# Kernel tuning notes

Measured on AMD Instinct MI355X. Metric: run time of the kernel, lower is better.

The kernel has to match this reference:

```python
import jax, jax.numpy as jnp
import numpy as np

N_NODES = 100000
N_EDGES = 1600000
MOTIF_DIM = 32
HIDDEN = 64


def setup_inputs() -> dict:
    key = jax.random.key(0)
    k1, k2, k3, k4 = jax.random.split(key, 4)
    motif_x = jax.random.normal(k1, (N_NODES, MOTIF_DIM), dtype=jnp.float32)
    edge_index = jax.random.randint(k2, (2, N_EDGES), 0, N_NODES, dtype=jnp.int64)
    in_dim = 4 * MOTIF_DIM
    W1 = jax.random.normal(k3, (in_dim, HIDDEN), dtype=jnp.float32) / np.sqrt(in_dim)
    b1 = jnp.zeros((HIDDEN,), dtype=jnp.float32)
    W2 = jax.random.normal(k4, (HIDDEN, 1), dtype=jnp.float32) / np.sqrt(HIDDEN)
    b2 = jnp.zeros((1,), dtype=jnp.float32)
    return {"motif_x": motif_x, "edge_index": edge_index, "W1": W1, "b1": b1, "W2": W2, "b2": b2}


def reference(motif_x, edge_index, W1, b1, W2, b2):
    src = edge_index[0]
    dst = edge_index[1]
    mu = motif_x[src]                      # [E, D] gather
    mv = motif_x[dst]                      # [E, D] gather
    feats = jnp.concatenate([mu, mv, jnp.abs(mu - mv), mu * mv], axis=1)  # [E, 4D]
    h = jax.nn.relu(feats @ W1 + b1)       # [E, H]
    g = jax.nn.sigmoid(h @ W2 + b2)[:, 0]  # [E]
    return jnp.clip(g, 0.0, 1.0)
```

## Files before the change

### kernel.cpp

```cpp
#include <hip/hip_runtime.h>

#define D 32
#define H 64

typedef __attribute__((ext_vector_type(8))) short bf16x8;
typedef __attribute__((ext_vector_type(4))) float f32x4;

union AB { uint4 u; bf16x8 v; };

__device__ __forceinline__ short f2bf_s(float f) {
  unsigned u = __float_as_uint(f);
  u += 0x7fffu + ((u >> 16) & 1u);
  return (short)(u >> 16);
}

__device__ __forceinline__ unsigned pack_bf2(float lo, float hi) {
  return __builtin_amdgcn_perm(__float_as_uint(hi), __float_as_uint(lo), 0x07060302u);
}

__global__ __launch_bounds__(256) void prep(
    const float* __restrict__ x, const float* __restrict__ W1,
    short* __restrict__ xbf, short* __restrict__ btab, int n4, int nPack) {
  int b = blockIdx.x;
  if (b < nPack) {
    int i = b * 256 + threadIdx.x;
    if (i < n4) {
      float4 v = ((const float4*)x)[i];
      short4 o;
      o.x = f2bf_s(v.x); o.y = f2bf_s(v.y); o.z = f2bf_s(v.z); o.w = f2bf_s(v.w);
      ((short4*)xbf)[i] = o;
    }
  } else {
    int id = (b - nPack) * 256 + threadIdx.x;
    if (id < 16 * 64 * 8) {
      int j = id & 7;
      int l = (id >> 3) & 63;
      int f = id >> 9;
      int s = f & 3, t = f >> 2;
      int k = s * 32 + (l >> 4) * 8 + j;
      int n = t * 16 + (l & 15);
      btab[id] = f2bf_s(W1[k * H + n]);
    }
  }
}

__device__ __forceinline__ void gather_tile(
    const uint4* __restrict__ xb, const int* __restrict__ ei,
    int tile, int m, int q, int nE, int nTiles, uint4& mu, uint4& mv) {
  int tc = tile < nTiles ? tile : nTiles - 1;
  int e  = tc * 16 + m;
  int ec = e < nE ? e : nE - 1;
  int s  = ei[ec];
  int d  = ei[ec + nE];
  mu = xb[s * 4 + q];
  mv = xb[d * 4 + q];
}

__device__ __forceinline__ void compute_tile(
    uint4 muU, uint4 mvU, const bf16x8* __restrict__ B,
    const f32x4* __restrict__ bias, const float* __restrict__ w2v, float bias2,
    int tile, int q, int m, int nE, float* __restrict__ out) {
  AB mu, mv, ac, ap;
  mu.u = muU; mv.u = mvU;
#pragma unroll
  for (int k = 0; k < 4; ++k) {
    unsigned a = (&mu.u.x)[k], b = (&mv.u.x)[k];
    float alo = __uint_as_float(a << 16);
    float ahi = __uint_as_float(a & 0xffff0000u);
    float blo = __uint_as_float(b << 16);
    float bhi = __uint_as_float(b & 0xffff0000u);
    float dlo = alo - blo, dhi = ahi - bhi;
    (&ac.u.x)[k] = pack_bf2(dlo, dhi) & 0x7fff7fffu;
    (&ap.u.x)[k] = pack_bf2(alo * blo, ahi * bhi);
  }

  float part[4];
#pragma unroll
  for (int t = 0; t < 4; ++t) {
    f32x4 acc = bias[t];
    acc = __builtin_amdgcn_mfma_f32_16x16x32_bf16(mu.v, B[t * 4 + 0], acc, 0, 0, 0);
    acc = __builtin_amdgcn_mfma_f32_16x16x32_bf16(mv.v, B[t * 4 + 1], acc, 0, 0, 0);
    acc = __builtin_amdgcn_mfma_f32_16x16x32_bf16(ac.v, B[t * 4 + 2], acc, 0, 0, 0);
    acc = __builtin_amdgcn_mfma_f32_16x16x32_bf16(ap.v, B[t * 4 + 3], acc, 0, 0, 0);
#pragma unroll
    for (int r = 0; r < 4; ++r) {
      float h = fmaxf(acc[r], 0.f);
      part[r] = (t == 0) ? h * w2v[0] : fmaf(h, w2v[t], part[r]);
    }
  }

#pragma unroll
  for (int mask = 1; mask < 16; mask <<= 1)
#pragma unroll
    for (int r = 0; r < 4; ++r)
      part[r] += __shfl_xor(part[r], mask, 64);

  if (m < 4) {
    int ew = tile * 16 + q * 4 + m;
    if (ew < nE) {
      float z = part[m] + bias2;
      float g = 1.f / (1.f + __expf(-z));
      out[ew] = fminf(fmaxf(g, 0.f), 1.f);
    }
  }
}

__global__ __launch_bounds__(256) void edge_mfma(
    const short* __restrict__ xbf, const short* __restrict__ btab,
    const int* __restrict__ ei,
    const float* __restrict__ b1, const float* __restrict__ W2,
    const float* __restrict__ b2, float* __restrict__ out,
    int nE, int nTiles) {
  int lane = threadIdx.x & 63;
  int wid  = (blockIdx.x * 256 + threadIdx.x) >> 6;
  int nW   = (gridDim.x * 256) >> 6;
  int m = lane & 15;
  int q = lane >> 4;

  bf16x8 B[16];
#pragma unroll
  for (int f = 0; f < 16; ++f)
    B[f] = *(const bf16x8*)(btab + (f * 64 + lane) * 8);

  f32x4 bias[4];
  float w2v[4];
#pragma unroll
  for (int t = 0; t < 4; ++t) {
    float bv = b1[t * 16 + m];
    bias[t] = (f32x4){bv, bv, bv, bv};
    w2v[t] = W2[t * 16 + m];
  }
  float bias2 = b2[0];

  const uint4* xb = (const uint4*)xbf;

  int t0 = wid, t1 = wid + nW;
  uint4 mu0, mv0, mu1, mv1;
  gather_tile(xb, ei, t0, m, q, nE, nTiles, mu0, mv0);
  gather_tile(xb, ei, t1, m, q, nE, nTiles, mu1, mv1);

  while (t0 < nTiles) {
    int n0 = t0 + 2 * nW, n1 = t1 + 2 * nW;
    uint4 pmu0, pmv0, pmu1, pmv1;
    gather_tile(xb, ei, n0, m, q, nE, nTiles, pmu0, pmv0);
    gather_tile(xb, ei, n1, m, q, nE, nTiles, pmu1, pmv1);

    compute_tile(mu0, mv0, B, bias, w2v, bias2, t0, q, m, nE, out);
    compute_tile(mu1, mv1, B, bias, w2v, bias2, t1, q, m, nE, out);

    mu0 = pmu0; mv0 = pmv0; mu1 = pmu1; mv1 = pmv1;
    t0 = n0; t1 = n1;
  }
}

__global__ __launch_bounds__(256) void edge_full(
    const float* __restrict__ x, const int* __restrict__ ei,
    const float* __restrict__ W1, const float* __restrict__ b1,
    const float* __restrict__ W2, const float* __restrict__ b2,
    float* __restrict__ out, int nE) {
  int e = blockIdx.x * 256 + threadIdx.x;
  if (e >= nE) return;
  int s = ei[e];
  int d = ei[e + nE];
  const float4* mu4 = (const float4*)(x + (size_t)s * D);
  const float4* mv4 = (const float4*)(x + (size_t)d * D);
  float mu[D], mv[D], c[D], p[D];
#pragma unroll
  for (int qq = 0; qq < D / 4; ++qq) {
    float4 a = mu4[qq];
    float4 b = mv4[qq];
    mu[4*qq+0] = a.x; mv[4*qq+0] = b.x; c[4*qq+0] = fabsf(a.x-b.x); p[4*qq+0] = a.x*b.x;
    mu[4*qq+1] = a.y; mv[4*qq+1] = b.y; c[4*qq+1] = fabsf(a.y-b.y); p[4*qq+1] = a.y*b.y;
    mu[4*qq+2] = a.z; mv[4*qq+2] = b.z; c[4*qq+2] = fabsf(a.z-b.z); p[4*qq+2] = a.z*b.z;
    mu[4*qq+3] = a.w; mv[4*qq+3] = b.w; c[4*qq+3] = fabsf(a.w-b.w); p[4*qq+3] = a.w*b.w;
  }
  float z = b2[0];
  for (int j = 0; j < H; ++j) {
    float a = b1[j];
#pragma unroll
    for (int k = 0; k < D; ++k) {
      a = fmaf(mu[k], W1[k * H + j], a);
      a = fmaf(mv[k], W1[(D + k) * H + j], a);
      a = fmaf(c[k],  W1[(2 * D + k) * H + j], a);
      a = fmaf(p[k],  W1[(3 * D + k) * H + j], a);
    }
    a = fmaxf(a, 0.f);
    z = fmaf(a, W2[j], z);
  }
  float g = 1.f / (1.f + __expf(-z));
  out[e] = fminf(fmaxf(g, 0.f), 1.f);
}

extern "C" void kernel_launch(void* const* d_in, const int* in_sizes, int n_in,
                              void* d_out, int out_size, void* d_ws, size_t ws_size,
                              hipStream_t stream) {
  const float* x  = (const float*)d_in[0];
  const int*   ei = (const int*)d_in[1];
  const float* W1 = (const float*)d_in[2];
  const float* b1 = (const float*)d_in[3];
  const float* W2 = (const float*)d_in[4];
  const float* b2 = (const float*)d_in[5];
  float* out = (float*)d_out;

  int nN = in_sizes[0] / D;
  int nE = in_sizes[1] / 2;

  size_t xbf_shorts = (size_t)nN * D;
  size_t need = (xbf_shorts + 16 * 64 * 8) * sizeof(short);
  if (ws_size >= need) {
    short* xbf  = (short*)d_ws;
    short* btab = xbf + xbf_shorts;
    int n4 = nN * D / 4;
    int nPack = (n4 + 255) / 256;
    int nBt = (16 * 64 * 8 + 255) / 256;
    prep<<<nPack + nBt, 256, 0, stream>>>(x, W1, xbf, btab, n4, nPack);
    int nTiles = (nE + 15) / 16;
    edge_mfma<<<2048, 256, 0, stream>>>(xbf, btab, ei, b1, W2, b2, out, nE, nTiles);
  } else {
    edge_full<<<(nE + 255) / 256, 256, 0, stream>>>(x, ei, W1, b1, W2, b2, out, nE);
  }
}
```

Measured before the change: 128.5 us.

## Restructure edge gather into 4-tile chunks with two-stage index/feature prefetch

Each wave now processes chunks of four 16-edge tiles. Edge indices are prefetched two chunks ahead and node features one chunk ahead, and each tile's feature loads are reissued right after that tile's compute. The aim is to keep more independent gathers in flight and to hide the dependent index-then-feature load latency. It also drops the redundant clamp after the sigmoid, keeps bias as scalars to save registers, and exits waves with no work early. The cost is higher register pressure from the 4-deep buffers, which may lower occupancy.

```diff
diff --git a/kernel.cpp b/kernel.cpp
--- a/kernel.cpp
+++ b/kernel.cpp
@@ -44,21 +44,9 @@
   }
 }
 
-__device__ __forceinline__ void gather_tile(
-    const uint4* __restrict__ xb, const int* __restrict__ ei,
-    int tile, int m, int q, int nE, int nTiles, uint4& mu, uint4& mv) {
-  int tc = tile < nTiles ? tile : nTiles - 1;
-  int e  = tc * 16 + m;
-  int ec = e < nE ? e : nE - 1;
-  int s  = ei[ec];
-  int d  = ei[ec + nE];
-  mu = xb[s * 4 + q];
-  mv = xb[d * 4 + q];
-}
-
 __device__ __forceinline__ void compute_tile(
     uint4 muU, uint4 mvU, const bf16x8* __restrict__ B,
-    const f32x4* __restrict__ bias, const float* __restrict__ w2v, float bias2,
+    const float* __restrict__ b1v, const float* __restrict__ w2v, float bias2,
     int tile, int q, int m, int nE, float* __restrict__ out) {
   AB mu, mv, ac, ap;
   mu.u = muU; mv.u = mvU;
@@ -77,7 +65,8 @@
   float part[4];
 #pragma unroll
   for (int t = 0; t < 4; ++t) {
-    f32x4 acc = bias[t];
+    float bv = b1v[t];
+    f32x4 acc = (f32x4){bv, bv, bv, bv};
     acc = __builtin_amdgcn_mfma_f32_16x16x32_bf16(mu.v, B[t * 4 + 0], acc, 0, 0, 0);
     acc = __builtin_amdgcn_mfma_f32_16x16x32_bf16(mv.v, B[t * 4 + 1], acc, 0, 0, 0);
     acc = __builtin_amdgcn_mfma_f32_16x16x32_bf16(ac.v, B[t * 4 + 2], acc, 0, 0, 0);
@@ -99,8 +88,7 @@
     int ew = tile * 16 + q * 4 + m;
     if (ew < nE) {
       float z = part[m] + bias2;
-      float g = 1.f / (1.f + __expf(-z));
-      out[ew] = fminf(fmaxf(g, 0.f), 1.f);
+      out[ew] = 1.f / (1.f + __expf(-z));
     }
   }
 }
@@ -116,40 +104,69 @@
   int nW   = (gridDim.x * 256) >> 6;
   int m = lane & 15;
   int q = lane >> 4;
+  int nChunks = (nTiles + 3) >> 2;
+  if (wid >= nChunks) return;
 
   bf16x8 B[16];
 #pragma unroll
   for (int f = 0; f < 16; ++f)
     B[f] = *(const bf16x8*)(btab + (f * 64 + lane) * 8);
 
-  f32x4 bias[4];
-  float w2v[4];
-#pragma unroll
-  for (int t = 0; t < 4; ++t) {
-    float bv = b1[t * 16 + m];
-    bias[t] = (f32x4){bv, bv, bv, bv};
+  float b1v[4], w2v[4];
+#pragma unroll
+  for (int t = 0; t < 4; ++t) {
+    b1v[t] = b1[t * 16 + m];
     w2v[t] = W2[t * 16 + m];
   }
   float bias2 = b2[0];
 
   const uint4* xb = (const uint4*)xbf;
-
-  int t0 = wid, t1 = wid + nW;
-  uint4 mu0, mv0, mu1, mv1;
-  gather_tile(xb, ei, t0, m, q, nE, nTiles, mu0, mv0);
-  gather_tile(xb, ei, t1, m, q, nE, nTiles, mu1, mv1);
-
-  while (t0 < nTiles) {
-    int n0 = t0 + 2 * nW, n1 = t1 + 2 * nW;
-    uint4 pmu0, pmv0, pmu1, pmv1;
-    gather_tile(xb, ei, n0, m, q, nE, nTiles, pmu0, pmv0);
-    gather_tile(xb, ei, n1, m, q, nE, nTiles, pmu1, pmv1);
-
-    compute_tile(mu0, mv0, B, bias, w2v, bias2, t0, q, m, nE, out);
-    compute_tile(mu1, mv1, B, bias, w2v, bias2, t1, q, m, nE, out);
-
-    mu0 = pmu0; mv0 = pmv0; mu1 = pmu1; mv1 = pmv1;
-    t0 = n0; t1 = n1;
+  int eLim = nE - 1;
+  int cLim = nChunks - 1;
+
+  int sn[4], dn[4], s2[4], d2[4];
+  uint4 amu[4], amv[4];
+
+  int c = wid;
+#pragma unroll
+  for (int t = 0; t < 4; ++t) {
+    int e = c * 64 + t * 16 + m; e = e < nE ? e : eLim;
+    sn[t] = ei[e]; dn[t] = ei[e + nE];
+  }
+#pragma unroll
+  for (int t = 0; t < 4; ++t) {
+    amu[t] = xb[sn[t] * 4 + q];
+    amv[t] = xb[dn[t] * 4 + q];
+  }
+  {
+    int cc = c + nW; cc = cc < nChunks ? cc : cLim;
+#pragma unroll
+    for (int t = 0; t < 4; ++t) {
+      int e = cc * 64 + t * 16 + m; e = e < nE ? e : eLim;
+      sn[t] = ei[e]; dn[t] = ei[e + nE];
+    }
+  }
+
+  while (c < nChunks) {
+    int cn = c + nW;
+    {
+      int cc = cn + nW; cc = cc < nChunks ? cc : cLim;
+#pragma unroll
+      for (int t = 0; t < 4; ++t) {
+        int e = cc * 64 + t * 16 + m; e = e < nE ? e : eLim;
+        s2[t] = ei[e]; d2[t] = ei[e + nE];
+      }
+    }
+#pragma unroll
+    for (int t = 0; t < 4; ++t) {
+      compute_tile(amu[t].x == 0xFFFFFFFFu && amu[t].y == 0xFFFFFFFFu ? amu[t] : amu[t],
+                   amv[t], B, b1v, w2v, bias2, c * 4 + t, q, m, nE, out);
+      amu[t] = xb[sn[t] * 4 + q];
+      amv[t] = xb[dn[t] * 4 + q];
+    }
+#pragma unroll
+    for (int t = 0; t < 4; ++t) { sn[t] = s2[t]; dn[t] = d2[t]; }
+    c = cn;
   }
 }
 
```

New measurement: 130.8 us. About the same (+1.8%).
